# Optimization experiments

Hardware: AMD Instinct MI355X
Metric: run time of the kernel (lower is better)

The kernel has to match this reference:

```python
import jax, jax.numpy as jnp
import numpy as np

B, S, E, H, F = 32, 512, 1024, 8, 8192
D = E // H  # head_dim = 128


def setup_inputs() -> dict:
    key = jax.random.key(0)
    ks = jax.random.split(key, 6)
    w = 0.02  # init scale
    return {
        "x": jax.random.normal(ks[0], (B, S, E), dtype=jnp.float32),
        "Wq": jax.random.normal(ks[1], (E, E), dtype=jnp.float32) * w,
        "bq": jnp.zeros((E,), dtype=jnp.float32),
        "Wk": jax.random.normal(ks[2], (E, E), dtype=jnp.float32) * w,
        "bk": jnp.zeros((E,), dtype=jnp.float32),
        "Wv": jax.random.normal(ks[3], (E, E), dtype=jnp.float32) * w,
        "bv": jnp.zeros((E,), dtype=jnp.float32),
        "W1": jax.random.normal(ks[4], (E, F), dtype=jnp.float32) * w,
        "b1": jnp.zeros((F,), dtype=jnp.float32),
        "W2": jax.random.normal(ks[5], (F, E), dtype=jnp.float32) * w,
        "b2": jnp.zeros((E,), dtype=jnp.float32),
    }


def reference(x, Wq, bq, Wk, bk, Wv, bv, W1, b1, W2, b2):
    b, s, e = x.shape
    h, d = H, e // H
    # headed projections: [b, h, s, d]
    q = (x @ Wq + bq).reshape(b, s, h, d).transpose(0, 2, 1, 3)
    k = (x @ Wk + bk).reshape(b, s, h, d).transpose(0, 2, 1, 3)
    v = (x @ Wv + bv).reshape(b, s, h, d).transpose(0, 2, 1, 3)
    # NOTE: original applies NO 1/sqrt(d) scaling
    scores = jnp.einsum("bhqd,bhkd->bhqk", q, k)
    attn = jax.nn.softmax(scores, axis=-1)
    o = jnp.einsum("bhqk,bhkd->bhqd", attn, v)
    o = o.transpose(0, 2, 1, 3).reshape(b, s, e)  # concat heads
    hid = jax.nn.gelu(o @ W1 + b1, approximate=False)  # nn.GELU default = exact erf
    return hid @ W2 + b2
```

## Files before the change

### kernel.cpp

```cpp
#include <hip/hip_runtime.h>
#include <hip/hip_bf16.h>
#include <math.h>

typedef __attribute__((ext_vector_type(8))) short bf16x8;
typedef __attribute__((ext_vector_type(4))) float f32x4;
typedef __hip_bfloat16 bf16;

__device__ __forceinline__ void gload_lds16(const void* g, void* l) {
  __builtin_amdgcn_global_load_lds((const __attribute__((address_space(1))) void*)g,
                                   (__attribute__((address_space(3))) void*)l,
                                   16, 0, 0);
}

__device__ __forceinline__ float gelu_erf(float x) {
  return 0.5f * x * (1.0f + erff(x * 0.70710678118654752f));
}

__global__ __launch_bounds__(256) void k_cvt_bf16(const float* __restrict__ in,
                                                  bf16* __restrict__ out, int n4) {
  int i = blockIdx.x * 256 + threadIdx.x;
  const int stride = gridDim.x * 256;
  for (; i < n4; i += stride) {
    float4 v = reinterpret_cast<const float4*>(in)[i];
    bf16* o = out + (size_t)i * 4;
    o[0] = __float2bfloat16(v.x);
    o[1] = __float2bfloat16(v.y);
    o[2] = __float2bfloat16(v.z);
    o[3] = __float2bfloat16(v.w);
  }
}

__global__ __launch_bounds__(256) void k_concat_bias(const float* __restrict__ bq,
                                                     const float* __restrict__ bk,
                                                     const float* __restrict__ bv,
                                                     float* __restrict__ cbias) {
  const int i = blockIdx.x * 256 + threadIdx.x;
  const float v = (i < 1024) ? bq[i] : (i < 2048) ? bk[i - 1024] : bv[i - 2048];
  cbias[i] = v;
}

__global__ __launch_bounds__(256) void k_transpose_w(const float* __restrict__ in,
                                                     bf16* __restrict__ out,
                                                     int R, int C) {
  __shared__ float tile[32][33];
  const int c0 = blockIdx.x * 32, r0 = blockIdx.y * 32;
  const int tx = threadIdx.x & 31, ty = threadIdx.x >> 5;
  for (int i = 0; i < 32; i += 8)
    tile[ty + i][tx] = in[(size_t)(r0 + ty + i) * C + c0 + tx];
  __syncthreads();
  for (int i = 0; i < 32; i += 8)
    out[(size_t)(c0 + ty + i) * R + r0 + tx] = __float2bfloat16(tile[tx][ty + i]);
}

__global__ __launch_bounds__(256) void k_transpose_v(const bf16* __restrict__ Vb,
                                                     bf16* __restrict__ Vt) {
  __shared__ bf16 tile[32][34];
  const int bh = blockIdx.z;
  const int b = bh >> 3, h = bh & 7;
  const int s0 = blockIdx.x * 32, d0 = blockIdx.y * 32;
  const int tx = threadIdx.x & 31, ty = threadIdx.x >> 5;
  for (int i = 0; i < 32; i += 8)
    tile[ty + i][tx] = Vb[((size_t)b * 512 + s0 + ty + i) * 1024 + h * 128 + d0 + tx];
  __syncthreads();
  for (int i = 0; i < 32; i += 8)
    Vt[((size_t)bh * 128 + d0 + ty + i) * 512 + s0 + tx] = tile[tx][ty + i];
}

template <int EPI, bool ACC>
__global__ __launch_bounds__(512, 2) void k_gemm256(
    const bf16* __restrict__ A, const bf16* __restrict__ Bt,
    const float* __restrict__ bias, void* __restrict__ Cout,
    int K, int lda, int ldb, int ldc) {
  __shared__ __attribute__((aligned(16))) char lds[131072];
  const int t = threadIdx.x, w = t >> 6, l = t & 63;
  const int gx = gridDim.x, nwg = gx * gridDim.y;
  int bid = blockIdx.y * gx + blockIdx.x;
  bid = (bid & 7) * (nwg >> 3) + (bid >> 3);
  const int bm = bid / gx, bn = bid % gx;
  const int wm = w >> 2, wn = w & 3;
  const int lq = l >> 4, lr = l & 15;

  const char* Ab = (const char*)(A + (size_t)(bm * 256) * lda);
  const char* Bb = (const char*)(Bt + (size_t)(bn * 256) * ldb);
  const int r0 = t >> 3, s0x = ((t & 7) ^ (r0 & 7)) << 4;
  const int r1 = (t + 512) >> 3, s1x = (((t + 512) & 7) ^ (r1 & 7)) << 4;
  const size_t la = (size_t)lda * 2, lb = (size_t)ldb * 2;
  const char* pA00 = Ab + (size_t)((r0 >> 6) * 128 + (r0 & 63)) * la + s0x;
  const char* pA10 = Ab + (size_t)((r1 >> 6) * 128 + (r1 & 63)) * la + s1x;
  const char* pA01 = Ab + (size_t)((r0 >> 6) * 128 + 64 + (r0 & 63)) * la + s0x;
  const char* pA11 = Ab + (size_t)((r1 >> 6) * 128 + 64 + (r1 & 63)) * la + s1x;
  const char* pB00 = Bb + (size_t)((r0 >> 5) * 64 + (r0 & 31)) * lb + s0x;
  const char* pB10 = Bb + (size_t)((r1 >> 5) * 64 + (r1 & 31)) * lb + s1x;
  const char* pB01 = Bb + (size_t)((r0 >> 5) * 64 + 32 + (r0 & 31)) * lb + s0x;
  const char* pB11 = Bb + (size_t)((r1 >> 5) * 64 + 32 + (r1 & 31)) * lb + s1x;

  const int swzb = (lq ^ (lr & 7)) << 4;
  const int aoff = wm * 8192 + lr * 128;
  const int boff = 32768 + wn * 4096 + lr * 128;

  f32x4 acc[8][4];
#pragma unroll
  for (int m = 0; m < 8; ++m)
#pragma unroll
    for (int n = 0; n < 4; ++n) acc[m][n] = (f32x4){0.f, 0.f, 0.f, 0.f};

#define ISSUE_A0(S) { gload_lds16(pA00, (S) + w * 1024); gload_lds16(pA10, (S) + 8192 + w * 1024); pA00 += 128; pA10 += 128; }
#define ISSUE_A1(S) { gload_lds16(pA01, (S) + 16384 + w * 1024); gload_lds16(pA11, (S) + 16384 + 8192 + w * 1024); pA01 += 128; pA11 += 128; }
#define ISSUE_B0(S) { gload_lds16(pB00, (S) + 32768 + w * 1024); gload_lds16(pB10, (S) + 32768 + 8192 + w * 1024); pB00 += 128; pB10 += 128; }
#define ISSUE_B1(S) { gload_lds16(pB01, (S) + 49152 + w * 1024); gload_lds16(pB11, (S) + 49152 + 8192 + w * 1024); pB01 += 128; pB11 += 128; }

  bf16x8 aF[4][2], bF01[2][2], bF23[2][2];
#define READ_A03(C) { _Pragma("unroll") for (int fr = 0; fr < 4; ++fr) _Pragma("unroll") for (int kk = 0; kk < 2; ++kk) aF[fr][kk] = *(const bf16x8*)((C) + aoff + fr * 2048 + (swzb ^ (kk << 6))); }
#define READ_A47(C) { _Pragma("unroll") for (int fr = 0; fr < 4; ++fr) _Pragma("unroll") for (int kk = 0; kk < 2; ++kk) aF[fr][kk] = *(const bf16x8*)((C) + 16384 + aoff + fr * 2048 + (swzb ^ (kk << 6))); }
#define READ_B01(C) { _Pragma("unroll") for (int fc = 0; fc < 2; ++fc) _Pragma("unroll") for (int kk = 0; kk < 2; ++kk) bF01[fc][kk] = *(const bf16x8*)((C) + boff + fc * 2048 + (swzb ^ (kk << 6))); }
#define READ_B23(C) { _Pragma("unroll") for (int fc = 0; fc < 2; ++fc) _Pragma("unroll") for (int kk = 0; kk < 2; ++kk) bF23[fc][kk] = *(const bf16x8*)((C) + 16384 + boff + fc * 2048 + (swzb ^ (kk << 6))); }

#define MFMA_Q(ACCR, BFR)                                               \
  { __builtin_amdgcn_s_setprio(1);                                      \
    _Pragma("unroll") for (int fr = 0; fr < 4; ++fr)                    \
      _Pragma("unroll") for (int fc = 0; fc < 2; ++fc)                  \
        _Pragma("unroll") for (int kk = 0; kk < 2; ++kk)                \
          acc[ACCR + fr][fc + ((&BFR == &bF23) ? 2 : 0)] =              \
              __builtin_amdgcn_mfma_f32_16x16x32_bf16(aF[fr][kk], BFR[fc][kk], acc[ACCR + fr][fc + ((&BFR == &bF23) ? 2 : 0)], 0, 0, 0); \
    __builtin_amdgcn_s_setprio(0); }

  ISSUE_A0(lds); ISSUE_B0(lds); ISSUE_B1(lds); ISSUE_A1(lds);

  const int NT = K >> 6;
  for (int kt = 0; kt < NT; ++kt) {
    char* cur = lds + (kt & 1) * 65536;
    char* nxt = lds + ((kt & 1) ^ 1) * 65536;
    const bool pre = (kt + 1 < NT);

    asm volatile("s_waitcnt vmcnt(4)" ::: "memory");
    __builtin_amdgcn_s_barrier();
    READ_A03(cur); READ_B01(cur);
    if (pre) ISSUE_A0(nxt);
    __builtin_amdgcn_s_barrier();
    MFMA_Q(0, bF01)
    if (pre) { asm volatile("s_waitcnt vmcnt(4)" ::: "memory"); }
    else     { asm volatile("s_waitcnt vmcnt(2)" ::: "memory"); }
    __builtin_amdgcn_s_barrier();

    READ_B23(cur);
    if (pre) ISSUE_B0(nxt);
    __builtin_amdgcn_s_barrier();
    MFMA_Q(0, bF23)
    if (pre) { asm volatile("s_waitcnt vmcnt(4)" ::: "memory"); }
    else     { asm volatile("s_waitcnt vmcnt(0)" ::: "memory"); }
    __builtin_amdgcn_s_barrier();

    READ_A47(cur);
    if (pre) ISSUE_B1(nxt);
    __builtin_amdgcn_s_barrier();
    MFMA_Q(4, bF01)
    __builtin_amdgcn_s_barrier();

    if (pre) ISSUE_A1(nxt);
    MFMA_Q(4, bF23)
  }
#undef ISSUE_A0
#undef ISSUE_A1
#undef ISSUE_B0
#undef ISSUE_B1
#undef READ_A03
#undef READ_A47
#undef READ_B01
#undef READ_B23
#undef MFMA_Q

  const int rowb = bm * 256 + wm * 128;
  const int colb = bn * 256 + wn * 64;
#pragma unroll
  for (int fr = 0; fr < 8; ++fr) {
#pragma unroll
    for (int fc = 0; fc < 4; ++fc) {
      const int col = colb + fc * 16 + lr;
      const float bv = bias ? bias[col] : 0.0f;
#pragma unroll
      for (int i = 0; i < 4; ++i) {
        const int row = rowb + fr * 16 + lq * 4 + i;
        float v = acc[fr][fc][i] + bv;
        if (EPI == 1) v = gelu_erf(v);
        if (EPI <= 1) {
          ((bf16*)Cout)[(size_t)row * ldc + col] = __float2bfloat16(v);
        } else if (EPI == 3) {
          bf16* Cq = (bf16*)Cout + (size_t)(colb >> 10) * 16777216ull;
          Cq[(size_t)row * 1024 + (col & 1023)] = __float2bfloat16(v);
        } else {
          float* Cf = (float*)Cout;
          const size_t idx = (size_t)row * ldc + col;
          if (ACC) v += Cf[idx];
          Cf[idx] = v;
        }
      }
    }
  }
}

__global__ __launch_bounds__(512, 1) void k_attn(const bf16* __restrict__ Qg,
                                                 const bf16* __restrict__ Kg,
                                                 const bf16* __restrict__ Vt,
                                                 bf16* __restrict__ Og) {
  __shared__ __attribute__((aligned(16))) char lds[131072];
  int bid = blockIdx.x;
  bid = (bid & 7) * 128 + (bid >> 3);
  const int bh = bid >> 2, q0 = (bid & 3) * 128;
  const int b = bh >> 3, h = bh & 7;
  const int t = threadIdx.x, w = t >> 6, l = t & 63;
  const int lq = l >> 4, lr = l & 15;
  const int wm = w >> 2, wn = w & 3;

  const int sr = t >> 4;
  const int ss = (t & 15) ^ (sr & 15);
  {
    const bf16* ks = Kg + ((size_t)b * 512 + sr) * 1024 + h * 128 + ss * 8;
#pragma unroll
    for (int j = 0; j < 16; ++j)
      gload_lds16(ks + (size_t)j * 32 * 1024, lds + j * 8192 + w * 1024);
  }

  bf16x8 qf[4][4];
  {
    const bf16* qb = Qg + ((size_t)b * 512 + q0 + wm * 64 + lr) * 1024 + h * 128 + lq * 8;
#pragma unroll
    for (int fr = 0; fr < 4; ++fr)
#pragma unroll
      for (int d0 = 0; d0 < 4; ++d0)
        qf[fr][d0] = *(const bf16x8*)(qb + (size_t)(fr * 16) * 1024 + d0 * 32);
  }

  asm volatile("s_waitcnt vmcnt(0)" ::: "memory");
  __builtin_amdgcn_s_barrier();
  asm volatile("" ::: "memory");

  f32x4 accS[4][8];
#pragma unroll
  for (int fr = 0; fr < 4; ++fr)
#pragma unroll
    for (int fc = 0; fc < 8; ++fc) accS[fr][fc] = (f32x4){0.f, 0.f, 0.f, 0.f};

  __builtin_amdgcn_s_setprio(1);
#pragma unroll
  for (int fc = 0; fc < 8; ++fc) {
    bf16x8 kf[4];
#pragma unroll
    for (int d0 = 0; d0 < 4; ++d0)
      kf[d0] = *(const bf16x8*)(lds + (wn * 128 + fc * 16 + lr) * 256 +
                                (((d0 * 4 + lq) ^ lr) << 4));
#pragma unroll
    for (int d0 = 0; d0 < 4; ++d0)
#pragma unroll
      for (int fr = 0; fr < 4; ++fr)
        accS[fr][fc] = __builtin_amdgcn_mfma_f32_16x16x32_bf16(qf[fr][d0], kf[d0], accS[fr][fc], 0, 0, 0);
  }
  __builtin_amdgcn_s_setprio(0);

  __builtin_amdgcn_s_barrier();
  asm volatile("" ::: "memory");

  const bf16* vs = Vt + ((size_t)bh * 128 + sr) * 512 + ss * 8;
#define IVC(kc, slot)                                                         \
  {                                                                           \
    _Pragma("unroll") for (int j = 0; j < 4; ++j)                             \
        gload_lds16(vs + (size_t)j * 32 * 512 + (kc) * 128,                   \
                    lds + (slot) * 32768 + j * 8192 + w * 1024);              \
  }
  IVC(0, 0)
  IVC(1, 1)

  float* redm = (float*)(lds + 98304);
  float* reds = (float*)(lds + 100352);
  float fm[4][4];
#pragma unroll
  for (int fr = 0; fr < 4; ++fr)
#pragma unroll
    for (int i = 0; i < 4; ++i) {
      float m = accS[fr][0][i];
#pragma unroll
      for (int fc = 1; fc < 8; ++fc) m = fmaxf(m, accS[fr][fc][i]);
      m = fmaxf(m, __shfl_xor(m, 1));
      m = fmaxf(m, __shfl_xor(m, 2));
      m = fmaxf(m, __shfl_xor(m, 4));
      m = fmaxf(m, __shfl_xor(m, 8));
      if (lr == 0) redm[wn * 128 + wm * 64 + fr * 16 + lq * 4 + i] = m;
    }
  asm volatile("s_waitcnt lgkmcnt(0)" ::: "memory");
  __builtin_amdgcn_s_barrier();
  asm volatile("" ::: "memory");
#pragma unroll
  for (int fr = 0; fr < 4; ++fr)
#pragma unroll
    for (int i = 0; i < 4; ++i) {
      const int row = wm * 64 + fr * 16 + lq * 4 + i;
      fm[fr][i] = fmaxf(fmaxf(redm[row], redm[128 + row]),
                        fmaxf(redm[256 + row], redm[384 + row]));
    }

  f32x4 oacc[4][2];
#pragma unroll
  for (int fr = 0; fr < 4; ++fr)
#pragma unroll
    for (int fc = 0; fc < 2; ++fc) oacc[fr][fc] = (f32x4){0.f, 0.f, 0.f, 0.f};
  float s4[4][4];
#pragma unroll
  for (int fr = 0; fr < 4; ++fr)
#pragma unroll
    for (int i = 0; i < 4; ++i) s4[fr][i] = 0.f;

#define EXPWRITE(kc)                                                           \
  if (wn == (kc)) {                                                            \
    _Pragma("unroll") for (int fr = 0; fr < 4; ++fr)                           \
      _Pragma("unroll") for (int i = 0; i < 4; ++i) {                          \
        const int row = wm * 64 + fr * 16 + lq * 4 + i;                        \
        const int rx = lq * 4 + i;                                             \
        _Pragma("unroll") for (int fc = 0; fc < 8; ++fc) {                     \
          const float e = __expf(accS[fr][fc][i] - fm[fr][i]);                 \
          s4[fr][i] += e;                                                      \
          *(unsigned short*)(lds + 65536 + row * 256 +                         \
                             (((fc * 2 + (lr >> 3)) ^ rx) << 4) + (lr & 7) * 2) = \
              __bfloat16_as_ushort(__float2bfloat16(e));                       \
        }                                                                      \
      }                                                                        \
  }

#define PVMFMA(kc)                                                             \
  {                                                                            \
    const char* Vb = lds + ((kc) & 1) * 32768;                                 \
    __builtin_amdgcn_s_setprio(1);                                             \
    _Pragma("unroll") for (int kk = 0; kk < 4; ++kk) {                         \
      bf16x8 pa[4], vb[2];                                                     \
      _Pragma("unroll") for (int fr = 0; fr < 4; ++fr)                         \
          pa[fr] = *(const bf16x8*)(lds + 65536 + (wm * 64 + fr * 16 + lr) * 256 + \
                                    (((kk * 4 + lq) ^ lr) << 4));              \
      _Pragma("unroll") for (int fc = 0; fc < 2; ++fc)                         \
          vb[fc] = *(const bf16x8*)(Vb + (wn * 32 + fc * 16 + lr) * 256 +      \
                                    (((kk * 4 + lq) ^ lr) << 4));              \
      _Pragma("unroll") for (int fr = 0; fr < 4; ++fr)                         \
        _Pragma("unroll") for (int fc = 0; fc < 2; ++fc)                       \
          oacc[fr][fc] = __builtin_amdgcn_mfma_f32_16x16x32_bf16(pa[fr], vb[fc], oacc[fr][fc], 0, 0, 0); \
    }                                                                          \
    __builtin_amdgcn_s_setprio(0);                                             \
  }

  EXPWRITE(0)
  asm volatile("s_waitcnt lgkmcnt(0)" ::: "memory");
  asm volatile("s_waitcnt vmcnt(4)" ::: "memory");
  __builtin_amdgcn_s_barrier();
  asm volatile("" ::: "memory");
  PVMFMA(0)
  __builtin_amdgcn_s_barrier();
  asm volatile("" ::: "memory");
  IVC(2, 0)
  EXPWRITE(1)
  asm volatile("s_waitcnt lgkmcnt(0)" ::: "memory");
  asm volatile("s_waitcnt vmcnt(4)" ::: "memory");
  __builtin_amdgcn_s_barrier();
  asm volatile("" ::: "memory");
  PVMFMA(1)
  __builtin_amdgcn_s_barrier();
  asm volatile("" ::: "memory");
  IVC(3, 1)
  EXPWRITE(2)
  asm volatile("s_waitcnt lgkmcnt(0)" ::: "memory");
  asm volatile("s_waitcnt vmcnt(4)" ::: "memory");
  __builtin_amdgcn_s_barrier();
  asm volatile("" ::: "memory");
  PVMFMA(2)
  __builtin_amdgcn_s_barrier();
  asm volatile("" ::: "memory");
  EXPWRITE(3)
  asm volatile("s_waitcnt lgkmcnt(0)" ::: "memory");
  asm volatile("s_waitcnt vmcnt(0)" ::: "memory");
  __builtin_amdgcn_s_barrier();
  asm volatile("" ::: "memory");
  PVMFMA(3)
#undef IVC
#undef EXPWRITE
#undef PVMFMA

#pragma unroll
  for (int fr = 0; fr < 4; ++fr)
#pragma unroll
    for (int i = 0; i < 4; ++i) {
      float s = s4[fr][i];
      s += __shfl_xor(s, 1);
      s += __shfl_xor(s, 2);
      s += __shfl_xor(s, 4);
      s += __shfl_xor(s, 8);
      if (lr == 0) reds[wn * 128 + wm * 64 + fr * 16 + lq * 4 + i] = s;
    }
  asm volatile("s_waitcnt lgkmcnt(0)" ::: "memory");
  __builtin_amdgcn_s_barrier();
  asm volatile("" ::: "memory");

#pragma unroll
  for (int fr = 0; fr < 4; ++fr)
#pragma unroll
    for (int i = 0; i < 4; ++i) {
      const int row = wm * 64 + fr * 16 + lq * 4 + i;
      const float rs = (reds[row] + reds[128 + row]) + (reds[256 + row] + reds[384 + row]);
#pragma unroll
      for (int fc = 0; fc < 2; ++fc) {
        const int col = wn * 32 + fc * 16 + lr;
        Og[((size_t)b * 512 + q0 + row) * 1024 + h * 128 + col] =
            __float2bfloat16(oacc[fr][fc][i] / rs);
      }
    }
}

extern "C" void kernel_launch(void* const* d_in, const int* in_sizes, int n_in,
                              void* d_out, int out_size, void* d_ws, size_t ws_size,
                              hipStream_t stream) {
  (void)in_sizes; (void)n_in; (void)out_size; (void)ws_size;
  const float* x  = (const float*)d_in[0];
  const float* Wq = (const float*)d_in[1];
  const float* bq = (const float*)d_in[2];
  const float* Wk = (const float*)d_in[3];
  const float* bk = (const float*)d_in[4];
  const float* Wv = (const float*)d_in[5];
  const float* bv = (const float*)d_in[6];
  const float* W1 = (const float*)d_in[7];
  const float* b1 = (const float*)d_in[8];
  const float* W2 = (const float*)d_in[9];
  const float* b2 = (const float*)d_in[10];
  float* out = (float*)d_out;
  char* ws = (char*)d_ws;
  constexpr size_t MB = 1ull << 20;

  bf16* XB  = (bf16*)(ws + 0);
  bf16* WQT = (bf16*)(ws + 32 * MB);
  bf16* WKT = (bf16*)(ws + 34 * MB);
  bf16* WVT = (bf16*)(ws + 36 * MB);
  bf16* W1T = (bf16*)(ws + 38 * MB);
  bf16* W2T = (bf16*)(ws + 54 * MB);
  bf16* OB  = (bf16*)(ws + 70 * MB);
  bf16* QB  = (bf16*)(ws + 102 * MB);
  bf16* KB  = (bf16*)(ws + 134 * MB);
  bf16* VB  = (bf16*)(ws + 166 * MB);
  bf16* VT  = (bf16*)(ws + 0);
  bf16* HC  = (bf16*)(ws + 102 * MB);
  float* CB = (float*)(ws + 70 * MB);

  k_cvt_bf16<<<2048, 256, 0, stream>>>(x, XB, (16384 * 1024) / 4);
  k_concat_bias<<<12, 256, 0, stream>>>(bq, bk, bv, CB);
  k_transpose_w<<<dim3(32, 32), 256, 0, stream>>>(Wq, WQT, 1024, 1024);
  k_transpose_w<<<dim3(32, 32), 256, 0, stream>>>(Wk, WKT, 1024, 1024);
  k_transpose_w<<<dim3(32, 32), 256, 0, stream>>>(Wv, WVT, 1024, 1024);
  k_transpose_w<<<dim3(256, 32), 256, 0, stream>>>(W1, W1T, 1024, 8192);
  k_transpose_w<<<dim3(32, 256), 256, 0, stream>>>(W2, W2T, 8192, 1024);

  k_gemm256<3, false><<<dim3(12, 64), 512, 0, stream>>>(XB, WQT, CB, QB, 1024, 1024, 1024, 1024);

  k_transpose_v<<<dim3(16, 4, 256), 256, 0, stream>>>(VB, VT);
  k_attn<<<1024, 512, 0, stream>>>(QB, KB, VT, OB);

  for (int chk = 0; chk < 4; ++chk) {
    k_gemm256<1, false><<<dim3(8, 64), 512, 0, stream>>>(
        OB, W1T + (size_t)chk * 2048 * 1024, b1 + chk * 2048, HC, 1024, 1024, 1024, 2048);
    if (chk == 0)
      k_gemm256<2, false><<<dim3(4, 64), 512, 0, stream>>>(
          HC, W2T + chk * 2048, b2, out, 2048, 2048, 8192, 1024);
    else
      k_gemm256<2, true><<<dim3(4, 64), 512, 0, stream>>>(
          HC, W2T + chk * 2048, nullptr, out, 2048, 2048, 8192, 1024);
  }
}
```

Baseline: 978.8 us.

## Shrink attention LDS footprint to fit multiple blocks per CU

The attention kernel's LDS footprint drops from 128KB to about 68KB so more than one block can be resident per CU, and the launch bound's minimum-occupancy hint goes from 1 to 4. To fit, K is staged into LDS in two halves with QK^T computed per half, and the V chunks are single-buffered rather than double-buffered, with a full vmcnt wait before each PV phase. This trades away V prefetch overlap and adds barriers in exchange for latency hiding across blocks. The stricter launch bound may also force register spills, given the large accumulator arrays.

New measurement: 1.095 ms. +11.8%, slower.

```diff
diff --git a/kernel.cpp b/kernel.cpp
--- a/kernel.cpp
+++ b/kernel.cpp
@@ -198,11 +198,11 @@
   }
 }
 
-__global__ __launch_bounds__(512, 1) void k_attn(const bf16* __restrict__ Qg,
+__global__ __launch_bounds__(512, 4) void k_attn(const bf16* __restrict__ Qg,
                                                  const bf16* __restrict__ Kg,
                                                  const bf16* __restrict__ Vt,
                                                  bf16* __restrict__ Og) {
-  __shared__ __attribute__((aligned(16))) char lds[131072];
+  __shared__ __attribute__((aligned(16))) char lds[69632];
   int bid = blockIdx.x;
   bid = (bid & 7) * 128 + (bid >> 3);
   const int bh = bid >> 2, q0 = (bid & 3) * 128;
@@ -213,12 +213,13 @@
 
   const int sr = t >> 4;
   const int ss = (t & 15) ^ (sr & 15);
-  {
-    const bf16* ks = Kg + ((size_t)b * 512 + sr) * 1024 + h * 128 + ss * 8;
-#pragma unroll
-    for (int j = 0; j < 16; ++j)
-      gload_lds16(ks + (size_t)j * 32 * 1024, lds + j * 8192 + w * 1024);
-  }
+
+  const bf16* ks = Kg + ((size_t)b * 512 + sr) * 1024 + h * 128 + ss * 8;
+#define STAGEK(hh)                                                            \
+  { _Pragma("unroll") for (int j = 0; j < 8; ++j)                             \
+      gload_lds16(ks + (size_t)((hh)*256 + j * 32) * 1024,                    \
+                  lds + j * 8192 + w * 1024); }
+  STAGEK(0)
 
   bf16x8 qf[4][4];
   {
@@ -240,38 +241,33 @@
 #pragma unroll
     for (int fc = 0; fc < 8; ++fc) accS[fr][fc] = (f32x4){0.f, 0.f, 0.f, 0.f};
 
-  __builtin_amdgcn_s_setprio(1);
-#pragma unroll
-  for (int fc = 0; fc < 8; ++fc) {
-    bf16x8 kf[4];
-#pragma unroll
-    for (int d0 = 0; d0 < 4; ++d0)
-      kf[d0] = *(const bf16x8*)(lds + (wn * 128 + fc * 16 + lr) * 256 +
-                                (((d0 * 4 + lq) ^ lr) << 4));
-#pragma unroll
-    for (int d0 = 0; d0 < 4; ++d0)
-#pragma unroll
-      for (int fr = 0; fr < 4; ++fr)
-        accS[fr][fc] = __builtin_amdgcn_mfma_f32_16x16x32_bf16(qf[fr][d0], kf[d0], accS[fr][fc], 0, 0, 0);
-  }
-  __builtin_amdgcn_s_setprio(0);
-
+#define QKH(hh)                                                               \
+  { __builtin_amdgcn_s_setprio(1);                                            \
+    _Pragma("unroll") for (int fc4 = 0; fc4 < 4; ++fc4) {                     \
+      bf16x8 kf[4];                                                           \
+      _Pragma("unroll") for (int d0 = 0; d0 < 4; ++d0)                        \
+        kf[d0] = *(const bf16x8*)(lds + (wn * 64 + fc4 * 16 + lr) * 256 +     \
+                                  (((d0 * 4 + lq) ^ lr) << 4));               \
+      _Pragma("unroll") for (int d0 = 0; d0 < 4; ++d0)                        \
+        _Pragma("unroll") for (int fr = 0; fr < 4; ++fr)                      \
+          accS[fr][(hh)*4 + fc4] = __builtin_amdgcn_mfma_f32_16x16x32_bf16(   \
+              qf[fr][d0], kf[d0], accS[fr][(hh)*4 + fc4], 0, 0, 0);           \
+    }                                                                         \
+    __builtin_amdgcn_s_setprio(0); }
+
+  QKH(0)
   __builtin_amdgcn_s_barrier();
   asm volatile("" ::: "memory");
-
-  const bf16* vs = Vt + ((size_t)bh * 128 + sr) * 512 + ss * 8;
-#define IVC(kc, slot)                                                         \
-  {                                                                           \
-    _Pragma("unroll") for (int j = 0; j < 4; ++j)                             \
-        gload_lds16(vs + (size_t)j * 32 * 512 + (kc) * 128,                   \
-                    lds + (slot) * 32768 + j * 8192 + w * 1024);              \
-  }
-  IVC(0, 0)
-  IVC(1, 1)
-
-  float* redm = (float*)(lds + 98304);
-  float* reds = (float*)(lds + 100352);
-  float fm[4][4];
+  STAGEK(1)
+  asm volatile("s_waitcnt vmcnt(0)" ::: "memory");
+  __builtin_amdgcn_s_barrier();
+  asm volatile("" ::: "memory");
+  QKH(1)
+#undef STAGEK
+#undef QKH
+
+  float* redm = (float*)(lds + 65536);
+  float* reds = (float*)(lds + 67584);
 #pragma unroll
   for (int fr = 0; fr < 4; ++fr)
 #pragma unroll
@@ -288,6 +284,15 @@
   asm volatile("s_waitcnt lgkmcnt(0)" ::: "memory");
   __builtin_amdgcn_s_barrier();
   asm volatile("" ::: "memory");
+
+  const bf16* vs = Vt + ((size_t)bh * 128 + sr) * 512 + ss * 8;
+#define IVC(kc)                                                               \
+  { _Pragma("unroll") for (int j = 0; j < 4; ++j)                             \
+      gload_lds16(vs + (size_t)(j * 32) * 512 + (kc)*128,                     \
+                  lds + j * 8192 + w * 1024); }
+  IVC(0)
+
+  float fm[4][4];
 #pragma unroll
   for (int fr = 0; fr < 4; ++fr)
 #pragma unroll
@@ -308,33 +313,33 @@
 #pragma unroll
     for (int i = 0; i < 4; ++i) s4[fr][i] = 0.f;
 
-#define EXPWRITE(kc)                                                           \
-  if (wn == (kc)) {                                                            \
+#define EXPWRITE(c)                                                            \
+  if ((wn >> 1) == ((c)&1)) {                                                  \
     _Pragma("unroll") for (int fr = 0; fr < 4; ++fr)                           \
       _Pragma("unroll") for (int i = 0; i < 4; ++i) {                          \
         const int row = wm * 64 + fr * 16 + lq * 4 + i;                        \
         const int rx = lq * 4 + i;                                             \
-        _Pragma("unroll") for (int fc = 0; fc < 8; ++fc) {                     \
-          const float e = __expf(accS[fr][fc][i] - fm[fr][i]);                 \
+        _Pragma("unroll") for (int j = 0; j < 4; ++j) {                        \
+          const float e = __expf(accS[fr][((c) >> 1) * 4 + j][i] - fm[fr][i]); \
           s4[fr][i] += e;                                                      \
-          *(unsigned short*)(lds + 65536 + row * 256 +                         \
-                             (((fc * 2 + (lr >> 3)) ^ rx) << 4) + (lr & 7) * 2) = \
+          const int cs = (wn & 1) * 8 + j * 2 + (lr >> 3);                     \
+          *(unsigned short*)(lds + 32768 + row * 256 + ((cs ^ rx) << 4) +      \
+                             (lr & 7) * 2) =                                   \
               __bfloat16_as_ushort(__float2bfloat16(e));                       \
         }                                                                      \
       }                                                                        \
   }
 
-#define PVMFMA(kc)                                                             \
+#define PVMFMA(c)                                                              \
   {                                                                            \
-    const char* Vb = lds + ((kc) & 1) * 32768;                                 \
     __builtin_amdgcn_s_setprio(1);                                             \
     _Pragma("unroll") for (int kk = 0; kk < 4; ++kk) {                         \
       bf16x8 pa[4], vb[2];                                                     \
       _Pragma("unroll") for (int fr = 0; fr < 4; ++fr)                         \
-          pa[fr] = *(const bf16x8*)(lds + 65536 + (wm * 64 + fr * 16 + lr) * 256 + \
+          pa[fr] = *(const bf16x8*)(lds + 32768 + (wm * 64 + fr * 16 + lr) * 256 + \
                                     (((kk * 4 + lq) ^ lr) << 4));              \
       _Pragma("unroll") for (int fc = 0; fc < 2; ++fc)                         \
-          vb[fc] = *(const bf16x8*)(Vb + (wn * 32 + fc * 16 + lr) * 256 +      \
+          vb[fc] = *(const bf16x8*)(lds + (wn * 32 + fc * 16 + lr) * 256 +     \
                                     (((kk * 4 + lq) ^ lr) << 4));              \
       _Pragma("unroll") for (int fr = 0; fr < 4; ++fr)                         \
         _Pragma("unroll") for (int fc = 0; fc < 2; ++fc)                       \
@@ -343,41 +348,27 @@
     __builtin_amdgcn_s_setprio(0);                                             \
   }
 
-  EXPWRITE(0)
-  asm volatile("s_waitcnt lgkmcnt(0)" ::: "memory");
-  asm volatile("s_waitcnt vmcnt(4)" ::: "memory");
-  __builtin_amdgcn_s_barrier();
-  asm volatile("" ::: "memory");
-  PVMFMA(0)
-  __builtin_amdgcn_s_barrier();
-  asm volatile("" ::: "memory");
-  IVC(2, 0)
-  EXPWRITE(1)
-  asm volatile("s_waitcnt lgkmcnt(0)" ::: "memory");
-  asm volatile("s_waitcnt vmcnt(4)" ::: "memory");
-  __builtin_amdgcn_s_barrier();
-  asm volatile("" ::: "memory");
-  PVMFMA(1)
-  __builtin_amdgcn_s_barrier();
-  asm volatile("" ::: "memory");
-  IVC(3, 1)
-  EXPWRITE(2)
-  asm volatile("s_waitcnt lgkmcnt(0)" ::: "memory");
-  asm volatile("s_waitcnt vmcnt(4)" ::: "memory");
-  __builtin_amdgcn_s_barrier();
-  asm volatile("" ::: "memory");
-  PVMFMA(2)
-  __builtin_amdgcn_s_barrier();
-  asm volatile("" ::: "memory");
-  EXPWRITE(3)
-  asm volatile("s_waitcnt lgkmcnt(0)" ::: "memory");
-  asm volatile("s_waitcnt vmcnt(0)" ::: "memory");
-  __builtin_amdgcn_s_barrier();
-  asm volatile("" ::: "memory");
-  PVMFMA(3)
+#define PVPHASE(c)                                                             \
+  EXPWRITE(c)                                                                  \
+  asm volatile("s_waitcnt lgkmcnt(0)" ::: "memory");                           \
+  asm volatile("s_waitcnt vmcnt(0)" ::: "memory");                             \
+  __builtin_amdgcn_s_barrier();                                                \
+  asm volatile("" ::: "memory");                                               \
+  PVMFMA(c)                                                                    \
+  __builtin_amdgcn_s_barrier();                                                \
+  asm volatile("" ::: "memory");
+
+  PVPHASE(0)
+  IVC(1)
+  PVPHASE(1)
+  IVC(2)
+  PVPHASE(2)
+  IVC(3)
+  PVPHASE(3)
 #undef IVC
 #undef EXPWRITE
 #undef PVMFMA
+#undef PVPHASE
 
 #pragma unroll
   for (int fr = 0; fr < 4; ++fr)
```

## Collapse GEMM main loop from four barrier-separated phases to two

Applied to the files above, without the earlier changes.

The K-loop of the bf16 MFMA GEMM used to alternate four small phases: read fragments, issue one prefetch, barrier, run a quarter of the MFMAs. Each K-step now runs two phases. Each phase reads A plus both B fragment halves at once, issues two prefetch groups, and runs a full half-tile of MFMAs. The vmcnt waits are adjusted to match. This cuts the per-iteration barriers from seven to two and gives the scheduler larger MFMA blocks, in exchange for coarser interleaving of global loads with compute and longer gaps between load issue and LDS reads.

New measurement: 973.8 us. No clear change (-0.5%).

```diff
diff --git a/kernel.cpp b/kernel.cpp
--- a/kernel.cpp
+++ b/kernel.cpp
@@ -115,13 +115,18 @@
 #define READ_B01(C) { _Pragma("unroll") for (int fc = 0; fc < 2; ++fc) _Pragma("unroll") for (int kk = 0; kk < 2; ++kk) bF01[fc][kk] = *(const bf16x8*)((C) + boff + fc * 2048 + (swzb ^ (kk << 6))); }
 #define READ_B23(C) { _Pragma("unroll") for (int fc = 0; fc < 2; ++fc) _Pragma("unroll") for (int kk = 0; kk < 2; ++kk) bF23[fc][kk] = *(const bf16x8*)((C) + 16384 + boff + fc * 2048 + (swzb ^ (kk << 6))); }
 
-#define MFMA_Q(ACCR, BFR)                                               \
+#define MFMA_HALF(ACCR)                                                 \
   { __builtin_amdgcn_s_setprio(1);                                      \
     _Pragma("unroll") for (int fr = 0; fr < 4; ++fr)                    \
       _Pragma("unroll") for (int fc = 0; fc < 2; ++fc)                  \
         _Pragma("unroll") for (int kk = 0; kk < 2; ++kk)                \
-          acc[ACCR + fr][fc + ((&BFR == &bF23) ? 2 : 0)] =              \
-              __builtin_amdgcn_mfma_f32_16x16x32_bf16(aF[fr][kk], BFR[fc][kk], acc[ACCR + fr][fc + ((&BFR == &bF23) ? 2 : 0)], 0, 0, 0); \
+          acc[ACCR + fr][fc] = __builtin_amdgcn_mfma_f32_16x16x32_bf16( \
+              aF[fr][kk], bF01[fc][kk], acc[ACCR + fr][fc], 0, 0, 0);   \
+    _Pragma("unroll") for (int fr = 0; fr < 4; ++fr)                    \
+      _Pragma("unroll") for (int fc = 0; fc < 2; ++fc)                  \
+        _Pragma("unroll") for (int kk = 0; kk < 2; ++kk)                \
+          acc[ACCR + fr][2 + fc] = __builtin_amdgcn_mfma_f32_16x16x32_bf16( \
+              aF[fr][kk], bF23[fc][kk], acc[ACCR + fr][2 + fc], 0, 0, 0); \
     __builtin_amdgcn_s_setprio(0); }
 
   ISSUE_A0(lds); ISSUE_B0(lds); ISSUE_B1(lds); ISSUE_A1(lds);
@@ -132,32 +137,18 @@
     char* nxt = lds + ((kt & 1) ^ 1) * 65536;
     const bool pre = (kt + 1 < NT);
 
-    asm volatile("s_waitcnt vmcnt(4)" ::: "memory");
+    asm volatile("s_waitcnt vmcnt(2)" ::: "memory");
     __builtin_amdgcn_s_barrier();
-    READ_A03(cur); READ_B01(cur);
-    if (pre) ISSUE_A0(nxt);
-    __builtin_amdgcn_s_barrier();
-    MFMA_Q(0, bF01)
-    if (pre) { asm volatile("s_waitcnt vmcnt(4)" ::: "memory"); }
-    else     { asm volatile("s_waitcnt vmcnt(2)" ::: "memory"); }
-    __builtin_amdgcn_s_barrier();
-
-    READ_B23(cur);
-    if (pre) ISSUE_B0(nxt);
-    __builtin_amdgcn_s_barrier();
-    MFMA_Q(0, bF23)
+    READ_A03(cur); READ_B01(cur); READ_B23(cur);
+    if (pre) { ISSUE_A0(nxt); ISSUE_B0(nxt); }
+    MFMA_HALF(0)
+
     if (pre) { asm volatile("s_waitcnt vmcnt(4)" ::: "memory"); }
     else     { asm volatile("s_waitcnt vmcnt(0)" ::: "memory"); }
     __builtin_amdgcn_s_barrier();
-
     READ_A47(cur);
-    if (pre) ISSUE_B1(nxt);
-    __builtin_amdgcn_s_barrier();
-    MFMA_Q(4, bF01)
-    __builtin_amdgcn_s_barrier();
-
-    if (pre) ISSUE_A1(nxt);
-    MFMA_Q(4, bF23)
+    if (pre) { ISSUE_B1(nxt); ISSUE_A1(nxt); }
+    MFMA_HALF(4)
   }
 #undef ISSUE_A0
 #undef ISSUE_A1
@@ -167,7 +158,7 @@
 #undef READ_A47
 #undef READ_B01
 #undef READ_B23
-#undef MFMA_Q
+#undef MFMA_HALF
 
   const int rowb = bm * 256 + wm * 128;
   const int colb = bn * 256 + wn * 64;
```
